# Performance work log

Hardware: AMD Instinct MI355X
Metric: run time of the kernel (lower is better)

Reference implementation:

```python
import jax, jax.numpy as jnp
import numpy as np

HIDDEN = 2048
INNER = 1024
NUM_EXPERTS = 64
TOP_K = 8
T_TOKENS = 512


def setup_inputs() -> dict:
    key = jax.random.key(0)
    k_x, k_gw, k_gb, k_w1, k_w2 = jax.random.split(key, 5)
    x = jax.random.normal(k_x, (T_TOKENS, HIDDEN), dtype=jnp.float32)
    gate_w = jax.random.normal(k_gw, (NUM_EXPERTS, HIDDEN), dtype=jnp.float32) * 0.02
    gate_b = jax.random.normal(k_gb, (NUM_EXPERTS,), dtype=jnp.float32) * 0.02
    # fc1: fused gate+up, [E, 2*INNER, HIDDEN]; fc2: down, [E, HIDDEN, INNER]
    w1 = jax.random.normal(k_w1, (NUM_EXPERTS, 2 * INNER, HIDDEN), dtype=jnp.float32) * 0.02
    w2 = jax.random.normal(k_w2, (NUM_EXPERTS, HIDDEN, INNER), dtype=jnp.float32) * 0.02
    return {"x": x, "gate_w": gate_w, "gate_b": gate_b, "w1": w1, "w2": w2}


def reference(x, gate_w, gate_b, w1, w2):
    # Router: ReplicatedLinear with bias -> logits [T, E]
    logits = x @ gate_w.T + gate_b
    # FusedMoE default routing: softmax (fp32), top-k, renormalize
    probs = jax.nn.softmax(logits.astype(jnp.float32), axis=-1)
    topk_w, topk_idx = jax.lax.top_k(probs, TOP_K)          # [T, K]
    topk_w = topk_w / jnp.sum(topk_w, axis=-1, keepdims=True)
    T, E = probs.shape
    # Sparse combine weights scattered into a dense [T, E] matrix
    combine = jnp.zeros((T, E), dtype=topk_w.dtype)
    combine = combine.at[jnp.arange(T)[:, None], topk_idx].add(topk_w)
    # Expert MLPs (dense-over-experts reference; combine zeros out unrouted pairs)
    h = jnp.einsum('th,eih->tei', x, w1)                    # [T, E, 2*INNER]
    gate_h, up_h = h[..., :INNER], h[..., INNER:]
    act = jax.nn.gelu(gate_h, approximate=True) * up_h      # gelu_pytorch_tanh
    y = jnp.einsum('tei,ehi->teh', act, w2)                 # [T, E, HIDDEN]
    # Weighted scatter-combine back to tokens
    return jnp.einsum('te,teh->th', combine.astype(x.dtype), y)
```

## Files before the change

kernel.cpp:

```cpp
#include <hip/hip_runtime.h>
#include <hip/hip_bf16.h>

#define HIDDEN 2048
#define INNER  1024
#define NE     64
#define TOPK   8
#define NTOK   512

typedef float f32x4 __attribute__((ext_vector_type(4)));
typedef short bf16x8 __attribute__((ext_vector_type(8)));

static __device__ __forceinline__ unsigned short b16(float f) {
  return __builtin_bit_cast(unsigned short, __float2bfloat16(f));
}
static __device__ __forceinline__ unsigned int pk2(float lo, float hi) {
  return (unsigned)b16(lo) | ((unsigned)b16(hi) << 16);
}

static __device__ __forceinline__ void decode_ce32(int flat, int& c, int& e) {
  int xcd = flat & 7, s = flat >> 3;
  c = s & 31;
  e = ((s >> 5) << 3) | xcd;
}

__global__ __launch_bounds__(256) void gating_kernel(
    const float* __restrict__ x, const float* __restrict__ gw, const float* __restrict__ gb,
    int* __restrict__ ticket, int* __restrict__ counts, int* __restrict__ offsets,
    int* __restrict__ topk_e, float* __restrict__ topk_w,
    int* __restrict__ perm_tok, float* __restrict__ perm_wt,
    unsigned short* __restrict__ xb, float* __restrict__ out) {
  const int t = blockIdx.x;
  const int tid = threadIdx.x;
  const int lane = tid & 63, w = tid >> 6;

  {
    const float4* xi = (const float4*)(x + (size_t)t * HIDDEN);
    float4 v0 = xi[tid * 2], v1 = xi[tid * 2 + 1];
    ushort4 o0, o1;
    o0.x = b16(v0.x); o0.y = b16(v0.y); o0.z = b16(v0.z); o0.w = b16(v0.w);
    o1.x = b16(v1.x); o1.y = b16(v1.y); o1.z = b16(v1.z); o1.w = b16(v1.w);
    ushort4* xo = (ushort4*)(xb + (size_t)t * HIDDEN);
    xo[tid * 2] = o0; xo[tid * 2 + 1] = o1;
    f32x4 z = (f32x4)0.f;
    f32x4* orow = (f32x4*)(out + (size_t)t * HIDDEN);
    orow[tid * 2] = z; orow[tid * 2 + 1] = z;
  }

  const int e = tid >> 2, seg = tid & 3;
  const f32x4* gr = (const f32x4*)(gw + (size_t)e * HIDDEN);
  const f32x4* xr = (const f32x4*)(x + (size_t)t * HIDDEN);
  float acc = 0.f;
  #pragma unroll 8
  for (int k = 0; k < 128; ++k) {
    int idx = k * 4 + seg;
    f32x4 a = xr[idx], b = gr[idx];
    acc += a.x * b.x + a.y * b.y + a.z * b.z + a.w * b.w;
  }
  acc += __shfl_xor(acc, 1);
  acc += __shfl_xor(acc, 2);
  __shared__ float sP[NE];
  if (seg == 0) sP[e] = acc;
  __syncthreads();

  __shared__ float sW[TOPK];
  __shared__ int   sE[TOPK];
  if (w == 0) {
    float logit = gb[lane] + sP[lane];
    float m = logit;
    #pragma unroll
    for (int off = 32; off; off >>= 1) m = fmaxf(m, __shfl_xor(m, off));
    float p = __expf(logit - m);
    float s = p;
    #pragma unroll
    for (int off = 32; off; off >>= 1) s += __shfl_xor(s, off);
    p /= s;
    float myp = p;
    #pragma unroll
    for (int k = 0; k < TOPK; ++k) {
      float v = myp; int ei = lane;
      #pragma unroll
      for (int off = 32; off; off >>= 1) {
        float v2 = __shfl_xor(v, off); int e2 = __shfl_xor(ei, off);
        if (v2 > v || (v2 == v && e2 < ei)) { v = v2; ei = e2; }
      }
      if (lane == 0) { sW[k] = v; sE[k] = ei; }
      if (lane == ei) myp = -1.0f;
    }
  }
  __syncthreads();
  if (tid < TOPK) {
    float ss = 0.f;
    #pragma unroll
    for (int k = 0; k < TOPK; ++k) ss += sW[k];
    topk_e[t * TOPK + tid] = sE[tid];
    topk_w[t * TOPK + tid] = sW[tid] / ss;
  }

  __threadfence();
  __syncthreads();
  __shared__ int slast;
  if (tid == 0) {
    int old = atomicAdd(ticket, 1);
    slast = (old == (int)gridDim.x - 1);
  }
  __syncthreads();
  if (!slast) return;
  __threadfence();

  __shared__ int hcnt[NE], soff[NE], ccur[NE];
  if (tid < NE) hcnt[tid] = 0;
  __syncthreads();
  for (int i = tid; i < NTOK * TOPK; i += 256) atomicAdd(&hcnt[topk_e[i]], 1);
  __syncthreads();
  if (tid < NE) {
    int c = hcnt[tid];
    int s = c;
    #pragma unroll
    for (int off = 1; off < 64; off <<= 1) {
      int o = __shfl_up(s, off);
      if (tid >= off) s += o;
    }
    soff[tid] = s - c; ccur[tid] = 0;
    counts[tid] = c; offsets[tid] = s - c;
  }
  __syncthreads();
  for (int i = tid; i < NTOK * TOPK; i += 256) {
    int ee = topk_e[i];
    int p = atomicAdd(&ccur[ee], 1);
    int pos = soff[ee] + p;
    perm_tok[pos] = i >> 3;
    perm_wt[pos] = topk_w[i];
  }
}

__global__ __launch_bounds__(256, 3) void phase1_kernel(
    const unsigned short* __restrict__ xb, const float* __restrict__ w1,
    const int* __restrict__ offsets, const int* __restrict__ counts,
    const int* __restrict__ perm_tok, unsigned short* __restrict__ act) {
  int c, e;
  decode_ce32(blockIdx.x, c, e);
  const int n_e = counts[e];
  if (n_e == 0) return;
  const int off = offsets[e];
  const int tid = threadIdx.x;
  const int lane = tid & 63, wave = tid >> 6;
  const int u2 = lane >> 4, l15 = lane & 15;
  const int mat = wave >> 1;
  const int wm  = (wave & 1) * 64;

  const int r16 = tid >> 4, l16 = tid & 15;
  const float* wg  = w1 + (size_t)e * (2 * INNER) * HIDDEN;
  const float* rp0 = wg + (size_t)(c * 32 + r16) * HIDDEN;
  const float* rp1 = rp0 + (size_t)16 * HIDDEN;
  const float* rp2 = wg + (size_t)(INNER + c * 32 + r16) * HIDDEN;
  const float* rp3 = rp2 + (size_t)16 * HIDDEN;
  const int bidx0 = r16 * 16 + (((l16 >> 1) ^ (r16 & 7)) << 1) + (l16 & 1);

  const int ar = tid >> 3, as = tid & 7;
  const int sxa = as ^ (ar & 7);

  __shared__ uint4 smem[2][1536];
  __shared__ int stok[128];
  float (*sU)[36] = (float(*)[36])&smem[0][0];

  for (int m0 = 0; m0 < n_e; m0 += 128) {
    __syncthreads();
    if (tid < 128) {
      int idx = m0 + tid;
      stok[tid] = perm_tok[off + (idx < n_e ? idx : n_e - 1)];
    }
    __syncthreads();

    const unsigned short* xr0 = xb + (size_t)stok[ar] * HIDDEN;
    const unsigned short* xr1 = xb + (size_t)stok[ar + 32] * HIDDEN;
    const unsigned short* xr2 = xb + (size_t)stok[ar + 64] * HIDDEN;
    const unsigned short* xr3 = xb + (size_t)stok[ar + 96] * HIDDEN;

    uint4 va0 = *((const uint4*)xr0 + as);
    uint4 va1 = *((const uint4*)xr1 + as);
    uint4 va2 = *((const uint4*)xr2 + as);
    uint4 va3 = *((const uint4*)xr3 + as);
    f32x4 vB0 = *((const f32x4*)rp0 + l16);
    f32x4 vB1 = *((const f32x4*)rp1 + l16);
    f32x4 vB2 = *((const f32x4*)rp2 + l16);
    f32x4 vB3 = *((const f32x4*)rp3 + l16);

    f32x4 acc[4][2];
    #pragma unroll
    for (int i = 0; i < 4; ++i)
      #pragma unroll
      for (int j = 0; j < 2; ++j) acc[i][j] = (f32x4)0.f;

    for (int k0 = 0; k0 < HIDDEN; k0 += 64) {
      const int cur = (k0 >> 6) & 1;
      uint4* A = smem[cur];
      A[ar * 8 + sxa]          = va0;
      A[(ar + 32) * 8 + sxa]   = va1;
      A[(ar + 64) * 8 + sxa]   = va2;
      A[(ar + 96) * 8 + sxa]   = va3;
      {
        uint2* bb = (uint2*)(smem[cur] + 1024);
        bb[bidx0]       = make_uint2(pk2(vB0.x, vB0.y), pk2(vB0.z, vB0.w));
        bb[bidx0 + 256] = make_uint2(pk2(vB1.x, vB1.y), pk2(vB1.z, vB1.w));
        bb[bidx0 + 512] = make_uint2(pk2(vB2.x, vB2.y), pk2(vB2.z, vB2.w));
        bb[bidx0 + 768] = make_uint2(pk2(vB3.x, vB3.y), pk2(vB3.z, vB3.w));
      }
      __syncthreads();
      int k1 = k0 + 64;
      if (k1 < HIDDEN) {
        va0 = *((const uint4*)(xr0 + k1) + as);
        va1 = *((const uint4*)(xr1 + k1) + as);
        va2 = *((const uint4*)(xr2 + k1) + as);
        va3 = *((const uint4*)(xr3 + k1) + as);
        vB0 = *((const f32x4*)(rp0 + k1) + l16);
        vB1 = *((const f32x4*)(rp1 + k1) + l16);
        vB2 = *((const f32x4*)(rp2 + k1) + l16);
        vB3 = *((const f32x4*)(rp3 + k1) + l16);
      }
      const uint4* Bq = smem[cur] + 1024;
      #pragma unroll
      for (int ks = 0; ks < 2; ++ks) {
        const int u = ks * 4 + u2;
        bf16x8 af[4], bfr[2];
        #pragma unroll
        for (int mi = 0; mi < 4; ++mi) {
          int r = wm + mi * 16 + l15;
          af[mi] = __builtin_bit_cast(bf16x8, A[r * 8 + (u ^ (r & 7))]);
        }
        #pragma unroll
        for (int ni = 0; ni < 2; ++ni) {
          int r = mat * 32 + ni * 16 + l15;
          bfr[ni] = __builtin_bit_cast(bf16x8, Bq[r * 8 + (u ^ (r & 7))]);
        }
        #pragma unroll
        for (int mi = 0; mi < 4; ++mi)
          #pragma unroll
          for (int ni = 0; ni < 2; ++ni)
            acc[mi][ni] = __builtin_amdgcn_mfma_f32_16x16x32_bf16(af[mi], bfr[ni], acc[mi][ni], 0, 0, 0);
      }
    }

    __syncthreads();
    if (mat == 1) {
      #pragma unroll
      for (int mi = 0; mi < 4; ++mi)
        #pragma unroll
        for (int ni = 0; ni < 2; ++ni)
          #pragma unroll
          for (int r4 = 0; r4 < 4; ++r4)
            sU[wm + mi * 16 + u2 * 4 + r4][ni * 16 + l15] = acc[mi][ni][r4];
    }
    __syncthreads();
    if (mat == 0) {
      #pragma unroll
      for (int mi = 0; mi < 4; ++mi)
        #pragma unroll
        for (int r4 = 0; r4 < 4; ++r4) {
          int mrow = wm + mi * 16 + u2 * 4 + r4;
          int m = m0 + mrow;
          if (m < n_e) {
            unsigned short* arow = act + (size_t)(off + m) * INNER + c * 32;
            #pragma unroll
            for (int ni = 0; ni < 2; ++ni) {
              int col = ni * 16 + l15;
              float g = acc[mi][ni][r4];
              float uu = sU[mrow][col];
              float ge = g / (1.0f + __expf(-1.5957691216057308f * (g + 0.044715f * g * g * g)));
              arow[col] = b16(ge * uu);
            }
          }
        }
    }
  }
}

__global__ __launch_bounds__(256, 3) void phase2_kernel(
    const unsigned short* __restrict__ act, const float* __restrict__ w2,
    const int* __restrict__ offsets, const int* __restrict__ counts,
    const int* __restrict__ perm_tok, const float* __restrict__ perm_wt,
    float* __restrict__ out) {
  int c, e;
  decode_ce32(blockIdx.x, c, e);
  const int n_e = counts[e];
  if (n_e == 0) return;
  const int off = offsets[e];
  const int tid = threadIdx.x;
  const int lane = tid & 63, wave = tid >> 6;
  const int u2 = lane >> 4, l15 = lane & 15;
  const int wm = wave * 32;

  const int r16 = tid >> 4, l16 = tid & 15;
  const float* rp0 = w2 + ((size_t)e * HIDDEN + c * 64 + r16) * INNER;
  const float* rp1 = rp0 + (size_t)16 * INNER;
  const float* rp2 = rp0 + (size_t)32 * INNER;
  const float* rp3 = rp0 + (size_t)48 * INNER;
  const int bidx0 = r16 * 16 + (((l16 >> 1) ^ (r16 & 7)) << 1) + (l16 & 1);

  const int ar = tid >> 3, as = tid & 7;
  const int sxa = as ^ (ar & 7);

  __shared__ uint4 smem[2][1536];
  __shared__ int   stok[128];
  __shared__ float swt[128];

  for (int m0 = 0; m0 < n_e; m0 += 128) {
    __syncthreads();
    if (tid < 128) {
      int idx = m0 + tid;
      int cl = idx < n_e ? idx : n_e - 1;
      stok[tid] = perm_tok[off + cl];
      swt[tid] = (idx < n_e) ? perm_wt[off + cl] : 0.f;
    }
    __syncthreads();

    const unsigned short* a0 = act + (size_t)(off + (m0 + ar      < n_e ? m0 + ar      : n_e - 1)) * INNER;
    const unsigned short* a1 = act + (size_t)(off + (m0 + ar + 32 < n_e ? m0 + ar + 32 : n_e - 1)) * INNER;
    const unsigned short* a2 = act + (size_t)(off + (m0 + ar + 64 < n_e ? m0 + ar + 64 : n_e - 1)) * INNER;
    const unsigned short* a3 = act + (size_t)(off + (m0 + ar + 96 < n_e ? m0 + ar + 96 : n_e - 1)) * INNER;

    uint4 va0 = *((const uint4*)a0 + as);
    uint4 va1 = *((const uint4*)a1 + as);
    uint4 va2 = *((const uint4*)a2 + as);
    uint4 va3 = *((const uint4*)a3 + as);
    f32x4 vB0 = *((const f32x4*)rp0 + l16);
    f32x4 vB1 = *((const f32x4*)rp1 + l16);
    f32x4 vB2 = *((const f32x4*)rp2 + l16);
    f32x4 vB3 = *((const f32x4*)rp3 + l16);

    f32x4 acc[2][4];
    #pragma unroll
    for (int i = 0; i < 2; ++i)
      #pragma unroll
      for (int j = 0; j < 4; ++j) acc[i][j] = (f32x4)0.f;

    for (int k0 = 0; k0 < INNER; k0 += 64) {
      const int cur = (k0 >> 6) & 1;
      uint4* A = smem[cur];
      A[ar * 8 + sxa]          = va0;
      A[(ar + 32) * 8 + sxa]   = va1;
      A[(ar + 64) * 8 + sxa]   = va2;
      A[(ar + 96) * 8 + sxa]   = va3;
      {
        uint2* bb = (uint2*)(smem[cur] + 1024);
        bb[bidx0]       = make_uint2(pk2(vB0.x, vB0.y), pk2(vB0.z, vB0.w));
        bb[bidx0 + 256] = make_uint2(pk2(vB1.x, vB1.y), pk2(vB1.z, vB1.w));
        bb[bidx0 + 512] = make_uint2(pk2(vB2.x, vB2.y), pk2(vB2.z, vB2.w));
        bb[bidx0 + 768] = make_uint2(pk2(vB3.x, vB3.y), pk2(vB3.z, vB3.w));
      }
      __syncthreads();
      int k1 = k0 + 64;
      if (k1 < INNER) {
        va0 = *((const uint4*)(a0 + k1) + as);
        va1 = *((const uint4*)(a1 + k1) + as);
        va2 = *((const uint4*)(a2 + k1) + as);
        va3 = *((const uint4*)(a3 + k1) + as);
        vB0 = *((const f32x4*)(rp0 + k1) + l16);
        vB1 = *((const f32x4*)(rp1 + k1) + l16);
        vB2 = *((const f32x4*)(rp2 + k1) + l16);
        vB3 = *((const f32x4*)(rp3 + k1) + l16);
      }
      const uint4* Bq = smem[cur] + 1024;
      #pragma unroll
      for (int ks = 0; ks < 2; ++ks) {
        const int u = ks * 4 + u2;
        bf16x8 af[2], bfr[4];
        #pragma unroll
        for (int mi = 0; mi < 2; ++mi) {
          int r = wm + mi * 16 + l15;
          af[mi] = __builtin_bit_cast(bf16x8, A[r * 8 + (u ^ (r & 7))]);
        }
        #pragma unroll
        for (int ni = 0; ni < 4; ++ni) {
          int r = ni * 16 + l15;
          bfr[ni] = __builtin_bit_cast(bf16x8, Bq[r * 8 + (u ^ (r & 7))]);
        }
        #pragma unroll
        for (int mi = 0; mi < 2; ++mi)
          #pragma unroll
          for (int ni = 0; ni < 4; ++ni)
            acc[mi][ni] = __builtin_amdgcn_mfma_f32_16x16x32_bf16(af[mi], bfr[ni], acc[mi][ni], 0, 0, 0);
      }
    }

    #pragma unroll
    for (int mi = 0; mi < 2; ++mi)
      #pragma unroll
      for (int r4 = 0; r4 < 4; ++r4) {
        int mrow = wm + mi * 16 + u2 * 4 + r4;
        int m = m0 + mrow;
        if (m < n_e) {
          int tok = stok[mrow];
          float wt = swt[mrow];
          float* orow = out + (size_t)tok * HIDDEN + c * 64;
          #pragma unroll
          for (int ni = 0; ni < 4; ++ni)
            atomicAdd(&orow[ni * 16 + l15], wt * acc[mi][ni][r4]);
        }
      }
    __syncthreads();
  }
}

extern "C" void kernel_launch(void* const* d_in, const int* in_sizes, int n_in,
                              void* d_out, int out_size, void* d_ws, size_t ws_size,
                              hipStream_t stream) {
  const float* x  = (const float*)d_in[0];
  const float* gw = (const float*)d_in[1];
  const float* gb = (const float*)d_in[2];
  const float* w1 = (const float*)d_in[3];
  const float* w2 = (const float*)d_in[4];
  float* out = (float*)d_out;

  char* ws = (char*)d_ws;
  int*   ticket   = (int*)(ws + 0x000);
  int*   counts   = (int*)(ws + 0x100);
  int*   offsets  = (int*)(ws + 0x200);
  int*   topk_e   = (int*)(ws + 0x1000);
  float* topk_w   = (float*)(ws + 0x5000);
  int*   perm_tok = (int*)(ws + 0x9000);
  float* perm_wt  = (float*)(ws + 0xD000);
  unsigned short* xb  = (unsigned short*)(ws + 0x11000);
  unsigned short* act = (unsigned short*)(ws + 0x220000);

  hipMemsetAsync(ticket, 0, 0x40, stream);

  gating_kernel<<<NTOK, 256, 0, stream>>>(x, gw, gb, ticket, counts, offsets,
                                          topk_e, topk_w, perm_tok, perm_wt, xb, out);
  phase1_kernel<<<2048, 256, 0, stream>>>(xb, w1, offsets, counts, perm_tok, act);
  phase2_kernel<<<2048, 256, 0, stream>>>(act, w2, offsets, counts, perm_tok, perm_wt, out);
}
```

Before: 436.0 us.

## Rewrite phase2 GEMM to load fragments directly from global without LDS staging

The down-projection kernel no longer stages activations and weights in shared memory with double buffering and barriers. Each wave now reads its bf16 activation fragments and fp32 weight rows straight from global memory into MFMA operands, converting the weights to bf16 in registers. Each block covers 128 output columns instead of 64, so the grid is halved. This removes LDS traffic and synchronisation, at the cost of more redundant global and L2 reads: all four waves reload the same activation rows, and the per-lane loads are narrow and strided. Register pressure also rises with the 8x2 accumulator tile.

```diff
diff --git a/kernel.cpp b/kernel.cpp
--- a/kernel.cpp
+++ b/kernel.cpp
@@ -21,6 +21,11 @@
   int xcd = flat & 7, s = flat >> 3;
   c = s & 31;
   e = ((s >> 5) << 3) | xcd;
+}
+static __device__ __forceinline__ void decode_ce16(int flat, int& c, int& e) {
+  int xcd = flat & 7, s = flat >> 3;
+  c = s & 15;
+  e = ((s >> 4) << 3) | xcd;
 }
 
 __global__ __launch_bounds__(256) void gating_kernel(
@@ -259,14 +264,14 @@
           int mrow = wm + mi * 16 + u2 * 4 + r4;
           int m = m0 + mrow;
           if (m < n_e) {
-            unsigned short* arow = act + (size_t)(off + m) * INNER + c * 32;
+            unsigned short* arw = act + (size_t)(off + m) * INNER + c * 32;
             #pragma unroll
             for (int ni = 0; ni < 2; ++ni) {
               int col = ni * 16 + l15;
               float g = acc[mi][ni][r4];
               float uu = sU[mrow][col];
               float ge = g / (1.0f + __expf(-1.5957691216057308f * (g + 0.044715f * g * g * g)));
-              arow[col] = b16(ge * uu);
+              arw[col] = b16(ge * uu);
             }
           }
         }
@@ -280,26 +285,18 @@
     const int* __restrict__ perm_tok, const float* __restrict__ perm_wt,
     float* __restrict__ out) {
   int c, e;
-  decode_ce32(blockIdx.x, c, e);
+  decode_ce16(blockIdx.x, c, e);
   const int n_e = counts[e];
   if (n_e == 0) return;
   const int off = offsets[e];
   const int tid = threadIdx.x;
   const int lane = tid & 63, wave = tid >> 6;
   const int u2 = lane >> 4, l15 = lane & 15;
-  const int wm = wave * 32;
-
-  const int r16 = tid >> 4, l16 = tid & 15;
-  const float* rp0 = w2 + ((size_t)e * HIDDEN + c * 64 + r16) * INNER;
-  const float* rp1 = rp0 + (size_t)16 * INNER;
-  const float* rp2 = rp0 + (size_t)32 * INNER;
-  const float* rp3 = rp0 + (size_t)48 * INNER;
-  const int bidx0 = r16 * 16 + (((l16 >> 1) ^ (r16 & 7)) << 1) + (l16 & 1);
-
-  const int ar = tid >> 3, as = tid & 7;
-  const int sxa = as ^ (ar & 7);
-
-  __shared__ uint4 smem[2][1536];
+  const int ncol0 = c * 128 + wave * 32;
+
+  const unsigned b_off0 = (unsigned)((e * HIDDEN + ncol0 + l15) * INNER + u2 * 8);
+  const unsigned b_off1 = b_off0 + 16u * INNER;
+
   __shared__ int   stok[128];
   __shared__ float swt[128];
 
@@ -313,91 +310,59 @@
     }
     __syncthreads();
 
-    const unsigned short* a0 = act + (size_t)(off + (m0 + ar      < n_e ? m0 + ar      : n_e - 1)) * INNER;
-    const unsigned short* a1 = act + (size_t)(off + (m0 + ar + 32 < n_e ? m0 + ar + 32 : n_e - 1)) * INNER;
-    const unsigned short* a2 = act + (size_t)(off + (m0 + ar + 64 < n_e ? m0 + ar + 64 : n_e - 1)) * INNER;
-    const unsigned short* a3 = act + (size_t)(off + (m0 + ar + 96 < n_e ? m0 + ar + 96 : n_e - 1)) * INNER;
-
-    uint4 va0 = *((const uint4*)a0 + as);
-    uint4 va1 = *((const uint4*)a1 + as);
-    uint4 va2 = *((const uint4*)a2 + as);
-    uint4 va3 = *((const uint4*)a3 + as);
-    f32x4 vB0 = *((const f32x4*)rp0 + l16);
-    f32x4 vB1 = *((const f32x4*)rp1 + l16);
-    f32x4 vB2 = *((const f32x4*)rp2 + l16);
-    f32x4 vB3 = *((const f32x4*)rp3 + l16);
-
-    f32x4 acc[2][4];
-    #pragma unroll
-    for (int i = 0; i < 2; ++i)
-      #pragma unroll
-      for (int j = 0; j < 4; ++j) acc[i][j] = (f32x4)0.f;
-
-    for (int k0 = 0; k0 < INNER; k0 += 64) {
-      const int cur = (k0 >> 6) & 1;
-      uint4* A = smem[cur];
-      A[ar * 8 + sxa]          = va0;
-      A[(ar + 32) * 8 + sxa]   = va1;
-      A[(ar + 64) * 8 + sxa]   = va2;
-      A[(ar + 96) * 8 + sxa]   = va3;
+    unsigned a_off[8];
+    #pragma unroll
+    for (int mf = 0; mf < 8; ++mf) {
+      int r = m0 + mf * 16 + l15;
+      a_off[mf] = (unsigned)((off + (r < n_e ? r : n_e - 1)) * INNER + u2 * 8);
+    }
+
+    f32x4 acc[8][2];
+    #pragma unroll
+    for (int i = 0; i < 8; ++i)
+      #pragma unroll
+      for (int j = 0; j < 2; ++j) acc[i][j] = (f32x4)0.f;
+
+    #pragma unroll 2
+    for (int k0 = 0; k0 < INNER; k0 += 32) {
+      bf16x8 af[8], bfr[2];
+      #pragma unroll
+      for (int mf = 0; mf < 8; ++mf)
+        af[mf] = *(const bf16x8*)(act + a_off[mf] + k0);
       {
-        uint2* bb = (uint2*)(smem[cur] + 1024);
-        bb[bidx0]       = make_uint2(pk2(vB0.x, vB0.y), pk2(vB0.z, vB0.w));
-        bb[bidx0 + 256] = make_uint2(pk2(vB1.x, vB1.y), pk2(vB1.z, vB1.w));
-        bb[bidx0 + 512] = make_uint2(pk2(vB2.x, vB2.y), pk2(vB2.z, vB2.w));
-        bb[bidx0 + 768] = make_uint2(pk2(vB3.x, vB3.y), pk2(vB3.z, vB3.w));
-      }
-      __syncthreads();
-      int k1 = k0 + 64;
-      if (k1 < INNER) {
-        va0 = *((const uint4*)(a0 + k1) + as);
-        va1 = *((const uint4*)(a1 + k1) + as);
-        va2 = *((const uint4*)(a2 + k1) + as);
-        va3 = *((const uint4*)(a3 + k1) + as);
-        vB0 = *((const f32x4*)(rp0 + k1) + l16);
-        vB1 = *((const f32x4*)(rp1 + k1) + l16);
-        vB2 = *((const f32x4*)(rp2 + k1) + l16);
-        vB3 = *((const f32x4*)(rp3 + k1) + l16);
-      }
-      const uint4* Bq = smem[cur] + 1024;
-      #pragma unroll
-      for (int ks = 0; ks < 2; ++ks) {
-        const int u = ks * 4 + u2;
-        bf16x8 af[2], bfr[4];
-        #pragma unroll
-        for (int mi = 0; mi < 2; ++mi) {
-          int r = wm + mi * 16 + l15;
-          af[mi] = __builtin_bit_cast(bf16x8, A[r * 8 + (u ^ (r & 7))]);
-        }
-        #pragma unroll
-        for (int ni = 0; ni < 4; ++ni) {
-          int r = ni * 16 + l15;
-          bfr[ni] = __builtin_bit_cast(bf16x8, Bq[r * 8 + (u ^ (r & 7))]);
-        }
-        #pragma unroll
-        for (int mi = 0; mi < 2; ++mi)
-          #pragma unroll
-          for (int ni = 0; ni < 4; ++ni)
-            acc[mi][ni] = __builtin_amdgcn_mfma_f32_16x16x32_bf16(af[mi], bfr[ni], acc[mi][ni], 0, 0, 0);
-      }
-    }
-
-    #pragma unroll
-    for (int mi = 0; mi < 2; ++mi)
+        f32x4 p0 = *(const f32x4*)(w2 + b_off0 + k0);
+        f32x4 p1 = *(const f32x4*)(w2 + b_off0 + k0 + 4);
+        uint4 u = { pk2(p0.x, p0.y), pk2(p0.z, p0.w), pk2(p1.x, p1.y), pk2(p1.z, p1.w) };
+        bfr[0] = __builtin_bit_cast(bf16x8, u);
+      }
+      {
+        f32x4 p0 = *(const f32x4*)(w2 + b_off1 + k0);
+        f32x4 p1 = *(const f32x4*)(w2 + b_off1 + k0 + 4);
+        uint4 u = { pk2(p0.x, p0.y), pk2(p0.z, p0.w), pk2(p1.x, p1.y), pk2(p1.z, p1.w) };
+        bfr[1] = __builtin_bit_cast(bf16x8, u);
+      }
+      #pragma unroll
+      for (int mf = 0; mf < 8; ++mf)
+        #pragma unroll
+        for (int ni = 0; ni < 2; ++ni)
+          acc[mf][ni] = __builtin_amdgcn_mfma_f32_16x16x32_bf16(af[mf], bfr[ni], acc[mf][ni], 0, 0, 0);
+    }
+
+    #pragma unroll
+    for (int mf = 0; mf < 8; ++mf)
       #pragma unroll
       for (int r4 = 0; r4 < 4; ++r4) {
-        int mrow = wm + mi * 16 + u2 * 4 + r4;
+        int mrow = mf * 16 + u2 * 4 + r4;
         int m = m0 + mrow;
         if (m < n_e) {
           int tok = stok[mrow];
           float wt = swt[mrow];
-          float* orow = out + (size_t)tok * HIDDEN + c * 64;
+          float* orow = out + (size_t)tok * HIDDEN + ncol0;
           #pragma unroll
-          for (int ni = 0; ni < 4; ++ni)
-            atomicAdd(&orow[ni * 16 + l15], wt * acc[mi][ni][r4]);
+          for (int ni = 0; ni < 2; ++ni)
+            atomicAdd(&orow[ni * 16 + l15], wt * acc[mf][ni][r4]);
         }
       }
-    __syncthreads();
   }
 }
 
@@ -427,5 +392,5 @@
   gating_kernel<<<NTOK, 256, 0, stream>>>(x, gw, gb, ticket, counts, offsets,
                                           topk_e, topk_w, perm_tok, perm_wt, xb, out);
   phase1_kernel<<<2048, 256, 0, stream>>>(xb, w1, offsets, counts, perm_tok, act);
-  phase2_kernel<<<2048, 256, 0, stream>>>(act, w2, offsets, counts, perm_tok, perm_wt, out);
-}
+  phase2_kernel<<<1024, 256, 0, stream>>>(act, w2, offsets, counts, perm_tok, perm_wt, out);
+}
```

Measured after the change: 569.1 us. 30.5% more time.
